# Performance work log

Measured on AMD Instinct MI355X. Metric: run time of the kernel, lower is better.

The kernel has to match this reference:

```python
import jax, jax.numpy as jnp
import numpy as np

B, Din, T, G = 8, 512, 1024, 128
DM, H, L, FF = 512, 8, 2, 2048
MAX_PERIOD = 10000.0


def _ln(x, s, b, eps=1e-5):
    m = x.mean(-1, keepdims=True)
    v = ((x - m) ** 2).mean(-1, keepdims=True)
    return (x - m) * jax.lax.rsqrt(v + eps) * s + b


def _rope(x, pos):
    # x: (B,H,S,Dh), pos: (S,)
    dh = x.shape[-1]
    half = dh // 2
    freqs = 1.0 / (MAX_PERIOD ** (jnp.arange(half, dtype=jnp.float32) / half))
    ang = pos[:, None] * freqs[None, :]              # (S, half)
    cos, sin = jnp.cos(ang), jnp.sin(ang)
    x1, x2 = x[..., :half], x[..., half:]
    return jnp.concatenate([x1 * cos - x2 * sin, x1 * sin + x2 * cos], axis=-1)


def _transformer(x, W_in, b_in, ln1_s, ln1_b, Wq, Wk, Wv, Wo, ls1,
                 ln2_s, ln2_b, W1, b1, W2, b2, ls2, lnf_s, lnf_b, W_out, b_out):
    # x: (B, Din, S) conv layout -> (B, S, DM)
    h = jnp.einsum('bds,de->bse', x, W_in) + b_in
    Bx, S, E = h.shape
    dh = E // H
    pos = jnp.arange(S, dtype=jnp.float32)
    scale = 1.0 / jnp.sqrt(jnp.asarray(dh, h.dtype))
    for l in range(Wq.shape[0]):
        y = _ln(h, ln1_s[l], ln1_b[l])
        q = (y @ Wq[l]).reshape(Bx, S, H, dh).transpose(0, 2, 1, 3)
        k = (y @ Wk[l]).reshape(Bx, S, H, dh).transpose(0, 2, 1, 3)
        v = (y @ Wv[l]).reshape(Bx, S, H, dh).transpose(0, 2, 1, 3)
        q, k = _rope(q, pos), _rope(k, pos)
        att = jax.nn.softmax(jnp.einsum('bhqd,bhkd->bhqk', q, k) * scale, axis=-1)
        o = jnp.einsum('bhqk,bhkd->bhqd', att, v).transpose(0, 2, 1, 3).reshape(Bx, S, E)
        h = h + ls1[l] * (o @ Wo[l])
        y = _ln(h, ln2_s[l], ln2_b[l])
        h = h + ls2[l] * (jax.nn.gelu(y @ W1[l] + b1[l]) @ W2[l] + b2[l])
    h = _ln(h, lnf_s, lnf_b)
    return (h @ W_out + b_out).transpose(0, 2, 1)  # (B, Din, S)


def _forward(features, alignment_matrix, num_segments_per_item, params):
    Bx, D, Tt = features.shape
    Gx = alignment_matrix.shape[1]
    ar_t = jnp.arange(Tt, dtype=jnp.int32)
    ar_g = jnp.arange(Gx, dtype=jnp.int32)
    group_mask = ar_g[None, :] < num_segments_per_item[:, None]          # (B,G)
    group_last = (alignment_matrix * ar_t.astype(features.dtype)).max(axis=2).astype(jnp.int32)  # (B,G)
    valid_last = jnp.where(group_mask, group_last, -1)
    frame_lengths = valid_last.max(axis=1) + 1                            # (B,)
    frame_mask = ar_t[None, :] < frame_lengths[:, None]                   # (B,T)
    last_for_count = jnp.where(group_mask, group_last, Tt + 1)
    num_q_before = jnp.sum(last_for_count[:, :, None] < ar_t[None, None, :], axis=1).astype(jnp.int32)  # (B,T)
    frame_dest = ar_t[None, :] + num_q_before                             # (B,T)
    query_dest = group_last + ar_g[None, :] + 1                           # (B,G)
    # mean-pooled query init
    summed = jnp.einsum('bgt,bdt->bgd', alignment_matrix, features)
    counts = jnp.maximum(alignment_matrix.sum(axis=2), 1.0)
    queries = (summed / counts[..., None]).transpose(0, 2, 1)             # (B,D,G)
    source_seq = jnp.concatenate([features, queries], axis=2)             # (B,D,T+G)
    dest = jnp.concatenate([frame_dest, query_dest], axis=1)              # (B,T+G)
    smask = jnp.concatenate([frame_mask, group_mask], axis=1)
    dest_m = jnp.where(smask, dest, Tt + Gx)
    perm = jnp.argsort(dest_m, axis=1)                                    # (B,T+G)
    interleaved = jnp.take_along_axis(source_seq, perm[:, None, :], axis=2)
    tout = _transformer(interleaved, *params)                             # (B,D,T+G)
    inv_perm = jnp.argsort(perm, axis=1)
    qpos = inv_perm[:, Tt:]                                               # (B,G)
    agg = jnp.take_along_axis(tout, qpos[:, None, :], axis=2)             # (B,D,G)
    return jnp.where(group_mask[:, None, :], agg, 0.0)


def setup_inputs() -> dict:
    key = jax.random.key(0)
    ks = jax.random.split(key, 8)
    rng = np.random.default_rng(0)
    align = np.zeros((B, G, T), np.float32)
    num_seg = np.zeros((B,), np.int32)
    for b in range(B):
        n = int(rng.integers(G // 2, G + 1))
        cuts = np.sort(rng.choice(np.arange(1, T), n - 1, replace=False))
        gid = np.searchsorted(cuts, np.arange(T), side='right')
        align[b, gid, np.arange(T)] = 1.0
        num_seg[b] = n
    s = 0.02
    return {
        'features': jax.random.normal(ks[0], (B, Din, T), jnp.float32),
        'alignment_matrix': jnp.asarray(align),
        'num_segments_per_item': jnp.asarray(num_seg),
        'W_in': jax.random.normal(ks[1], (Din, DM), jnp.float32) * s,
        'b_in': jnp.zeros((DM,), jnp.float32),
        'ln1_s': jnp.ones((L, DM), jnp.float32), 'ln1_b': jnp.zeros((L, DM), jnp.float32),
        'Wq': jax.random.normal(ks[2], (L, DM, DM), jnp.float32) * s,
        'Wk': jax.random.normal(ks[3], (L, DM, DM), jnp.float32) * s,
        'Wv': jax.random.normal(ks[4], (L, DM, DM), jnp.float32) * s,
        'Wo': jax.random.normal(ks[5], (L, DM, DM), jnp.float32) * s,
        'ls1': 0.01 * jnp.ones((L, DM), jnp.float32),
        'ln2_s': jnp.ones((L, DM), jnp.float32), 'ln2_b': jnp.zeros((L, DM), jnp.float32),
        'W1': jax.random.normal(ks[6], (L, DM, FF), jnp.float32) * s,
        'b1': jnp.zeros((L, FF), jnp.float32),
        'W2': jax.random.normal(ks[7], (L, FF, DM), jnp.float32) * s,
        'b2': jnp.zeros((L, DM), jnp.float32),
        'ls2': 0.01 * jnp.ones((L, DM), jnp.float32),
        'lnf_s': jnp.ones((DM,), jnp.float32), 'lnf_b': jnp.zeros((DM,), jnp.float32),
        'W_out': jax.random.normal(jax.random.fold_in(key, 9), (DM, Din), jnp.float32) * s,
        'b_out': jnp.zeros((Din,), jnp.float32),
    }


def reference(features, alignment_matrix, num_segments_per_item, W_in, b_in, ln1_s, ln1_b,
              Wq, Wk, Wv, Wo, ls1, ln2_s, ln2_b, W1, b1, W2, b2, ls2, lnf_s, lnf_b, W_out, b_out):
    params = (W_in, b_in, ln1_s, ln1_b, Wq, Wk, Wv, Wo, ls1,
              ln2_s, ln2_b, W1, b1, W2, b2, ls2, lnf_s, lnf_b, W_out, b_out)
    return _forward(features, alignment_matrix, num_segments_per_item, params)
```

## Files before the change

### kernel.cpp

```cpp
#include <hip/hip_runtime.h>
#include <hip/hip_bf16.h>
#include <math.h>

#define NB   8
#define NT   1024
#define NG   128
#define NS   1152
#define NDIN 512
#define NDM  512
#define NH   8
#define NDH  64
#define NFF  2048
#define NL   2

typedef __attribute__((ext_vector_type(4))) float  floatx4;
typedef __attribute__((ext_vector_type(8))) short  shortx8;

__device__ __forceinline__ float gelu_f(float x) {
    float u = 1.5957691216057308f * (x + 0.044715f * x * x * x);
    return x / (1.0f + __expf(-u));
}

__device__ __forceinline__ void gload_lds16(const void* g, void* l) {
    __builtin_amdgcn_global_load_lds((const __attribute__((address_space(1))) unsigned int*)g,
                                     (__attribute__((address_space(3))) unsigned int*)l, 16, 0, 0);
}

__device__ __forceinline__ short f2bfs(float x) {
    __hip_bfloat16 h = __float2bfloat16(x);
    return *(short*)&h;
}
__device__ __forceinline__ unsigned pack_bf2_rz(float a, float b) {
    unsigned au = *(unsigned*)&a, bu = *(unsigned*)&b;
    return (au >> 16) | (bu & 0xFFFF0000u);
}

__device__ __forceinline__ void swzxy(int& bx, int& by, int gx, int gy) {
    const int nwg = gx * gy;
    int flat = by * gx + bx;
    if ((nwg & 7) == 0) flat = (flat & 7) * (nwg >> 3) + (flat >> 3);
    bx = flat % gx; by = flat / gx;
}

__device__ __forceinline__ void wtile(const float* __restrict__ src,
        __hip_bfloat16* __restrict__ dst, int K, int N, int i, int tid, short tile[32][33])
{
    const int gx = N / 32;
    const int n0 = (i % gx) * 32;
    const int k0 = (i / gx) * 32;
    {
        const int r = tid >> 3, c4 = (tid & 7) * 4;
        float4 v = *(const float4*)&src[(size_t)(k0 + r) * N + n0 + c4];
        tile[c4 + 0][r] = f2bfs(v.x);
        tile[c4 + 1][r] = f2bfs(v.y);
        tile[c4 + 2][r] = f2bfs(v.z);
        tile[c4 + 3][r] = f2bfs(v.w);
    }
    __syncthreads();
    {
        const int r = tid >> 3, c4 = (tid & 7) * 4;
        short* dp = (short*)dst + (size_t)(n0 + r) * K + k0 + c4;
        short4 v;
        v.x = tile[r][c4 + 0]; v.y = tile[r][c4 + 1];
        v.z = tile[r][c4 + 2]; v.w = tile[r][c4 + 3];
        *(short4*)dp = v;
    }
}

__global__ __launch_bounds__(256) void prep0_k(
        float2* __restrict__ tab,
        const float* __restrict__ features, float* __restrict__ featT,
        const float* W_in, const float* Wq, const float* Wk, const float* Wv,
        const float* Wo, const float* W1, const float* W2, const float* W_out,
        __hip_bfloat16* w_inT, __hip_bfloat16* wqkvT0, __hip_bfloat16* wqkvT1,
        __hip_bfloat16* woT0, __hip_bfloat16* woT1,
        __hip_bfloat16* w1T0, __hip_bfloat16* w1T1,
        __hip_bfloat16* w2T0, __hip_bfloat16* w2T1, __hip_bfloat16* woutT)
{
    __shared__ __align__(16) char smem[32 * 33 * 4];
    const int tid = threadIdx.x;
    const int blk = blockIdx.x;
    if (blk < 144) {
        const int idx = blk * 256 + tid;
        const int s = idx >> 5, i = idx & 31;
        const float fr = __expf(-(float)i * 0.28782313662425576f);
        const float ang = (float)s * fr;
        tab[idx] = make_float2(cosf(ang), sinf(ang));
    } else if (blk < 144 + 4096) {
        float (*tile)[33] = (float(*)[33])smem;
        const int v = blk - 144;
        const int t0 = (v & 31) * 32;
        const int d0 = ((v >> 5) & 15) * 32;
        const int b  = v >> 9;
        const int r = tid >> 3, c4 = (tid & 7) * 4;
        {
            float4 w = *(const float4*)&features[((size_t)(b * NDIN + d0 + r)) * NT + t0 + c4];
            tile[c4 + 0][r] = w.x; tile[c4 + 1][r] = w.y;
            tile[c4 + 2][r] = w.z; tile[c4 + 3][r] = w.w;
        }
        __syncthreads();
        {
            float4 w;
            w.x = tile[r][c4 + 0]; w.y = tile[r][c4 + 1];
            w.z = tile[r][c4 + 2]; w.w = tile[r][c4 + 3];
            *(float4*)&featT[((size_t)(b * NT + t0 + r)) * NDIN + d0 + c4] = w;
        }
    } else {
        short (*tile)[33] = (short(*)[33])smem;
        const int i = blk - (144 + 4096);
        const float* src; __hip_bfloat16* dst; int K, N, ti;
        if (i < 256) { src = W_in; dst = w_inT; K = 512; N = 512; ti = i; }
        else if (i < 6400) {
            int r = i - 256;
            const int l = r / 3072; r -= l * 3072;
            const size_t o5 = (size_t)l * 262144, o2 = (size_t)l * 1048576;
            if (r < 256)       { src = Wq + o5; dst = (l ? wqkvT1 : wqkvT0);          K = 512;  N = 512;  ti = r; }
            else if (r < 512)  { src = Wk + o5; dst = (l ? wqkvT1 : wqkvT0) + 262144; K = 512;  N = 512;  ti = r - 256; }
            else if (r < 768)  { src = Wv + o5; dst = (l ? wqkvT1 : wqkvT0) + 524288; K = 512;  N = 512;  ti = r - 512; }
            else if (r < 1024) { src = Wo + o5; dst = (l ? woT1 : woT0);              K = 512;  N = 512;  ti = r - 768; }
            else if (r < 2048) { src = W1 + o2; dst = (l ? w1T1 : w1T0);              K = 512;  N = 2048; ti = r - 1024; }
            else               { src = W2 + o2; dst = (l ? w2T1 : w2T0);              K = 2048; N = 512;  ti = r - 2048; }
        }
        else { src = W_out; dst = woutT; K = 512; N = 512; ti = i - 6400; }
        wtile(src, dst, K, N, ti, tid, tile);
    }
}

__global__ __launch_bounds__(256) void pool_k(const float* __restrict__ align,
        const float* __restrict__ featT, int* __restrict__ glast,
        float* __restrict__ queries)
{
    __shared__ float redf[256];
    __shared__ int   redi[256];
    __shared__ float aw[NT];
    const int bg = blockIdx.x;
    const int b = bg >> 7;
    const int tid = threadIdx.x;
    const float* arow = align + (size_t)bg * NT;
    float cnt = 0.f, last = 0.f;
    int tmin = NT;
    for (int t = tid; t < NT; t += 256) {
        float a = arow[t];
        cnt += a;
        last = fmaxf(last, a * (float)t);
        if (a > 0.f) tmin = min(tmin, t);
    }
    redf[tid] = cnt; __syncthreads();
    for (int s = 128; s > 0; s >>= 1) { if (tid < s) redf[tid] += redf[tid + s]; __syncthreads(); }
    float c = redf[0]; __syncthreads();
    redf[tid] = last; __syncthreads();
    for (int s = 128; s > 0; s >>= 1) { if (tid < s) redf[tid] = fmaxf(redf[tid], redf[tid + s]); __syncthreads(); }
    float l = redf[0];
    redi[tid] = tmin; __syncthreads();
    for (int s = 128; s > 0; s >>= 1) { if (tid < s) redi[tid] = min(redi[tid], redi[tid + s]); __syncthreads(); }
    const int t0 = redi[0];
    const int t1 = (int)l;
    if (tid == 0) glast[bg] = t1;
    __syncthreads();
    for (int t = t0 + tid; t <= t1; t += 256) aw[t - t0] = arow[t];
    __syncthreads();
    const float invc = 1.0f / fmaxf(c, 1.0f);
    const float* fT = featT + (size_t)b * NT * NDIN;
    for (int d = tid; d < NDIN; d += 256) {
        float s = 0.f;
        for (int t = t0; t <= t1; ++t) s += aw[t - t0] * fT[(size_t)t * NDIN + d];
        queries[(size_t)bg * NDIN + d] = s * invc;
    }
}

__global__ __launch_bounds__(256) void rank_k(const int* __restrict__ glast,
        const int* __restrict__ nsegp, int* __restrict__ perm, int* __restrict__ qpos)
{
    __shared__ int dm[NS];
    __shared__ int gl[NG];
    const int b = blockIdx.y;
    const int tid = threadIdx.x;
    const int j = blockIdx.x * 256 + tid;
    if (tid < NG) gl[tid] = glast[b * NG + tid];
    const int ns = nsegp[b];
    __syncthreads();
    for (int jj = tid; jj < NS; jj += 256) {
        int d;
        if (jj < NT) {
            int t = jj, nq = 0, flen = 0;
            for (int g = 0; g < ns; ++g) {
                flen = max(flen, gl[g] + 1);
                nq += (gl[g] < t) ? 1 : 0;
            }
            d = (t < flen) ? (t + nq) : NS;
        } else {
            int g = jj - NT;
            d = (g < ns) ? (gl[g] + g + 1) : NS;
        }
        dm[jj] = d;
    }
    __syncthreads();
    if (j < NS) {
        const int my = dm[j];
        int r = 0;
        for (int t = 0; t < NS; ++t) {
            int v2 = dm[t];
            r += (v2 < my || (v2 == my && t < j)) ? 1 : 0;
        }
        perm[b * NS + r] = j;
        if (j >= NT) qpos[b * NG + (j - NT)] = r;
    }
}

__global__ __launch_bounds__(256) void buildx_k(const float* __restrict__ featT,
        const float* __restrict__ queries, const int* __restrict__ perm,
        __hip_bfloat16* __restrict__ X)
{
    const int idx = blockIdx.x * 256 + threadIdx.x;
    if (idx >= NB * NS * (NDIN / 4)) return;
    const int dq = idx & 127;
    const int p = (idx >> 7) % NS;
    const int b = idx / (NS * 128);
    const int j = perm[b * NS + p];
    const float4* src = (j < NT)
        ? (const float4*)&featT[((size_t)(b * NT + j)) * NDIN]
        : (const float4*)&queries[((size_t)(b * NG + (j - NT))) * NDIN];
    float4 v = src[dq];
    short4 o;
    o.x = f2bfs(v.x); o.y = f2bfs(v.y); o.z = f2bfs(v.z); o.w = f2bfs(v.w);
    *(short4*)((short*)X + ((size_t)(b * NS + p)) * NDIN + dq * 4) = o;
}

__global__ __launch_bounds__(256) void bgemmw1_k(const __hip_bfloat16* __restrict__ A,
        const __hip_bfloat16* __restrict__ Bt, __hip_bfloat16* __restrict__ Cout,
        const float* __restrict__ bias, int M, int N, int K)
{
    __shared__ __align__(16) short SM[4][128 * 32];
    const int tid = threadIdx.x;
    const int wave = tid >> 6, lane = tid & 63;
    const int quad = lane >> 4, l16 = lane & 15;
    const int wm = wave >> 1, wn = wave & 1;
    int bx = blockIdx.x, by = blockIdx.y;
    swzxy(bx, by, gridDim.x, gridDim.y);
    const size_t bm = (size_t)by * 128, bn = (size_t)bx * 128;
    const int sw = (l16 >> 1) & 3;
    const short* Ag = (const short*)A;
    const short* Bg = (const short*)Bt;
    const int lrow = lane >> 2;
    const int lchunk = (lane & 3) ^ ((lane >> 3) & 3);
    const int rS = wave * 32;

    floatx4 acc[4][4];
#pragma unroll
    for (int i = 0; i < 4; ++i)
#pragma unroll
        for (int j = 0; j < 4; ++j) acc[i][j] = (floatx4){0.f, 0.f, 0.f, 0.f};

    {
        const size_t ra = (bm + rS + lrow) * (size_t)K + lchunk * 8;
        const size_t rb = (bn + rS + lrow) * (size_t)K + lchunk * 8;
        gload_lds16(Ag + ra,                    &SM[0][rS * 32]);
        gload_lds16(Ag + ra + 16 * (size_t)K,   &SM[0][(rS + 16) * 32]);
        gload_lds16(Bg + rb,                    &SM[2][rS * 32]);
        gload_lds16(Bg + rb + 16 * (size_t)K,   &SM[2][(rS + 16) * 32]);
    }
    __syncthreads();
    int cur = 0;
    for (int k0 = 0; k0 < K; k0 += 32) {
        if (k0 + 32 < K) {
            const int nx = cur ^ 1;
            const size_t ra = (bm + rS + lrow) * (size_t)K + (k0 + 32) + lchunk * 8;
            const size_t rb = (bn + rS + lrow) * (size_t)K + (k0 + 32) + lchunk * 8;
            gload_lds16(Ag + ra,                  &SM[nx][rS * 32]);
            gload_lds16(Ag + ra + 16 * (size_t)K, &SM[nx][(rS + 16) * 32]);
            gload_lds16(Bg + rb,                  &SM[2 + nx][rS * 32]);
            gload_lds16(Bg + rb + 16 * (size_t)K, &SM[2 + nx][(rS + 16) * 32]);
        }
        shortx8 af[4], bf[4];
#pragma unroll
        for (int t = 0; t < 4; ++t) {
            af[t] = *(const shortx8*)&SM[cur][(wm * 64 + t * 16 + l16) * 32 + ((quad ^ sw) * 8)];
            bf[t] = *(const shortx8*)&SM[2 + cur][(wn * 64 + t * 16 + l16) * 32 + ((quad ^ sw) * 8)];
        }
#pragma unroll
        for (int mt = 0; mt < 4; ++mt)
#pragma unroll
            for (int nt = 0; nt < 4; ++nt)
                acc[mt][nt] = __builtin_amdgcn_mfma_f32_16x16x32_bf16(af[mt], bf[nt], acc[mt][nt], 0, 0, 0);
        __syncthreads();
        cur ^= 1;
    }
    const size_t mbase = bm + wm * 64;
    const size_t nbase = bn + wn * 64;
    short* ep = &SM[wave][0];
#pragma unroll
    for (int nt = 0; nt < 4; ++nt) {
        const size_t n = nbase + nt * 16 + l16;
        const float bz = bias[n];
        const int col = nt * 16 + l16;
#pragma unroll
        for (int mt = 0; mt < 4; ++mt)
#pragma unroll
            for (int r = 0; r < 4; ++r) {
                const int rl = mt * 16 + quad * 4 + r;
                float e = gelu_f(acc[mt][nt][r] + bz);
                ep[rl * 64 + (((col >> 3) ^ (rl & 7)) * 8) + (col & 7)] = f2bfs(e);
            }
    }
    __asm__ __volatile__("" ::: "memory");
#pragma unroll
    for (int c2 = 0; c2 < 8; ++c2) {
        const int rl = c2 * 8 + (lane >> 3);
        const int cc = lane & 7;
        shortx8 v = *(const shortx8*)&ep[rl * 64 + ((cc ^ (rl & 7)) * 8)];
        *(shortx8*)((short*)Cout + (mbase + rl) * N + nbase + cc * 8) = v;
    }
}

__global__ __launch_bounds__(256) void bgemmqkv_k(const __hip_bfloat16* __restrict__ A,
        const __hip_bfloat16* __restrict__ Bt, __hip_bfloat16* __restrict__ qh,
        __hip_bfloat16* __restrict__ kh, __hip_bfloat16* __restrict__ vT,
        const float2* __restrict__ tab)
{
    __shared__ __align__(16) short SM[4][128 * 32];
    const int tid = threadIdx.x;
    const int wave = tid >> 6, lane = tid & 63;
    const int quad = lane >> 4, l16 = lane & 15;
    const int wm = wave >> 1, wn = wave & 1;
    int bx = blockIdx.x, by = blockIdx.y;
    swzxy(bx, by, gridDim.x, gridDim.y);
    const size_t bm = (size_t)by * 128, bn = (size_t)bx * 128;
    const int sw = (l16 >> 1) & 3;
    const int K = 512;
    const short* Ag = (const short*)A;
    const short* Bg = (const short*)Bt;
    const int lrow = lane >> 2;
    const int lchunk = (lane & 3) ^ ((lane >> 3) & 3);
    const int rS = wave * 32;

    floatx4 acc[4][4];
#pragma unroll
    for (int i = 0; i < 4; ++i)
#pragma unroll
        for (int j = 0; j < 4; ++j) acc[i][j] = (floatx4){0.f, 0.f, 0.f, 0.f};

    {
        const size_t ra = (bm + rS + lrow) * (size_t)K + lchunk * 8;
        const size_t rb = (bn + rS + lrow) * (size_t)K + lchunk * 8;
        gload_lds16(Ag + ra,                  &SM[0][rS * 32]);
        gload_lds16(Ag + ra + 16 * (size_t)K, &SM[0][(rS + 16) * 32]);
        gload_lds16(Bg + rb,                  &SM[2][rS * 32]);
        gload_lds16(Bg + rb + 16 * (size_t)K, &SM[2][(rS + 16) * 32]);
    }
    __syncthreads();
    int cur = 0;
    for (int k0 = 0; k0 < K; k0 += 32) {
        if (k0 + 32 < K) {
            const int nx = cur ^ 1;
            const size_t ra = (bm + rS + lrow) * (size_t)K + (k0 + 32) + lchunk * 8;
            const size_t rb = (bn + rS + lrow) * (size_t)K + (k0 + 32) + lchunk * 8;
            gload_lds16(Ag + ra,                  &SM[nx][rS * 32]);
            gload_lds16(Ag + ra + 16 * (size_t)K, &SM[nx][(rS + 16) * 32]);
            gload_lds16(Bg + rb,                  &SM[2 + nx][rS * 32]);
            gload_lds16(Bg + rb + 16 * (size_t)K, &SM[2 + nx][(rS + 16) * 32]);
        }
        shortx8 af[4], bf[4];
#pragma unroll
        for (int t = 0; t < 4; ++t) {
            af[t] = *(const shortx8*)&SM[cur][(wm * 64 + t * 16 + l16) * 32 + ((quad ^ sw) * 8)];
            bf[t] = *(const shortx8*)&SM[2 + cur][(wn * 64 + t * 16 + l16) * 32 + ((quad ^ sw) * 8)];
        }
#pragma unroll
        for (int mt = 0; mt < 4; ++mt)
#pragma unroll
            for (int nt = 0; nt < 4; ++nt)
                acc[mt][nt] = __builtin_amdgcn_mfma_f32_16x16x32_bf16(af[mt], bf[nt], acc[mt][nt], 0, 0, 0);
        __syncthreads();
        cur ^= 1;
    }
    short* ep = &SM[wave][0];
    const int bidx = (int)(bm / NS);
    const int sbase = (int)(bm - (size_t)bidx * NS) + wm * 64;
    const int region = (int)(bn >> 9);
    if (region < 2) {
        const float qsc = region ? 1.0f : 0.18033688011112043f;
        const int h = (int)((((int)bn & 511) + wn * 64) >> 6);
#pragma unroll
        for (int nt = 0; nt < 2; ++nt) {
            const int d1 = nt * 16 + l16, d2 = d1 + 32;
            const float2* tp = tab + d1;
#pragma unroll
            for (int mt = 0; mt < 4; ++mt)
#pragma unroll
                for (int r = 0; r < 4; ++r) {
                    const int sl = mt * 16 + quad * 4 + r;
                    const int s = sbase + sl;
                    float x1 = acc[mt][nt][r], x2 = acc[mt][nt + 2][r];
                    float2 cs = tp[s * 32];
                    ep[sl * 64 + (((d1 >> 3) ^ (sl & 7)) * 8) + (d1 & 7)] = f2bfs(qsc * (x1 * cs.x - x2 * cs.y));
                    ep[sl * 64 + (((d2 >> 3) ^ (sl & 7)) * 8) + (d2 & 7)] = f2bfs(qsc * (x1 * cs.y + x2 * cs.x));
                }
        }
        __asm__ __volatile__("" ::: "memory");
        short* dst = (short*)(region ? kh : qh) + ((size_t)(bidx * NH + h)) * NS * NDH;
#pragma unroll
        for (int c2 = 0; c2 < 8; ++c2) {
            const int sl = c2 * 8 + (lane >> 3);
            const int cc = lane & 7;
            shortx8 v = *(const shortx8*)&ep[sl * 64 + ((cc ^ (sl & 7)) * 8)];
            *(shortx8*)(dst + (size_t)(sbase + sl) * NDH + cc * 8) = v;
        }
    } else {
        const int base = (int)(bn - 1024) + wn * 64;
        const int h = base >> 6;
#pragma unroll
        for (int nt = 0; nt < 4; ++nt) {
            const int dl = nt * 16 + l16;
#pragma unroll
            for (int mt = 0; mt < 4; ++mt)
#pragma unroll
                for (int r = 0; r < 4; ++r) {
                    const int sl = mt * 16 + quad * 4 + r;
                    ep[dl * 64 + (((sl >> 3) ^ (dl & 7)) * 8) + (sl & 7)] = f2bfs(acc[mt][nt][r]);
                }
        }
        __asm__ __volatile__("" ::: "memory");
        short* vp = (short*)vT + ((size_t)(bidx * NH + h)) * NDH * NS;
#pragma unroll
        for (int c2 = 0; c2 < 8; ++c2) {
            const int dl = c2 * 8 + (lane >> 3);
            const int cc = lane & 7;
            shortx8 v = *(const shortx8*)&ep[dl * 64 + ((cc ^ (dl & 7)) * 8)];
            *(shortx8*)(vp + (size_t)dl * NS + sbase + cc * 8) = v;
        }
    }
}

template <int EPI>
__global__ __launch_bounds__(256) void bgemm64_k(const __hip_bfloat16* __restrict__ A,
        const __hip_bfloat16* __restrict__ Bt, void* __restrict__ Cout,
        const float* __restrict__ bias, const float* __restrict__ ls,
        const float* __restrict__ res, const int* __restrict__ nsegp, int M, int N, int K)
{
    __shared__ __align__(16) short As[2][64 * 32];
    __shared__ __align__(16) short Bs[2][128 * 32];
    const int tid = threadIdx.x;
    const int wave = tid >> 6, lane = tid & 63;
    const int quad = lane >> 4, l16 = lane & 15;
    const int wm = wave >> 1, wn = wave & 1;
    int bx = blockIdx.x, by = blockIdx.y;
    swzxy(bx, by, gridDim.x, gridDim.y);
    const size_t bm = (size_t)by * 64, bn = (size_t)bx * 128;
    const int sw = (l16 >> 1) & 3;
    const short* Ag = (const short*)A;
    const short* Bg = (const short*)Bt;
    const int lrow = lane >> 2;
    const int lchunk = (lane & 3) ^ ((lane >> 3) & 3);
    const int rA = wave * 16, rB = wave * 32;

    floatx4 acc[2][4];
#pragma unroll
    for (int i = 0; i < 2; ++i)
#pragma unroll
        for (int j = 0; j < 4; ++j) acc[i][j] = (floatx4){0.f, 0.f, 0.f, 0.f};

    {
        const size_t ra = (bm + rA + lrow) * (size_t)K + lchunk * 8;
        const size_t rb = (bn + rB + lrow) * (size_t)K + lchunk * 8;
        gload_lds16(Ag + ra,                  &As[0][rA * 32]);
        gload_lds16(Bg + rb,                  &Bs[0][rB * 32]);
        gload_lds16(Bg + rb + 16 * (size_t)K, &Bs[0][(rB + 16) * 32]);
    }
    __syncthreads();
    int cur = 0;
    for (int k0 = 0; k0 < K; k0 += 32) {
        if (k0 + 32 < K) {
            const int nx = cur ^ 1;
            const size_t ra = (bm + rA + lrow) * (size_t)K + (k0 + 32) + lchunk * 8;
            const size_t rb = (bn + rB + lrow) * (size_t)K + (k0 + 32) + lchunk * 8;
            gload_lds16(Ag + ra,                  &As[nx][rA * 32]);
            gload_lds16(Bg + rb,                  &Bs[nx][rB * 32]);
            gload_lds16(Bg + rb + 16 * (size_t)K, &Bs[nx][(rB + 16) * 32]);
        }
        shortx8 af[2], bf[4];
#pragma unroll
        for (int t = 0; t < 2; ++t)
            af[t] = *(const shortx8*)&As[cur][(wm * 32 + t * 16 + l16) * 32 + ((quad ^ sw) * 8)];
#pragma unroll
        for (int t = 0; t < 4; ++t)
            bf[t] = *(const shortx8*)&Bs[cur][(wn * 64 + t * 16 + l16) * 32 + ((quad ^ sw) * 8)];
#pragma unroll
        for (int mt = 0; mt < 2; ++mt)
#pragma unroll
            for (int nt = 0; nt < 4; ++nt)
                acc[mt][nt] = __builtin_amdgcn_mfma_f32_16x16x32_bf16(af[mt], bf[nt], acc[mt][nt], 0, 0, 0);
        __syncthreads();
        cur ^= 1;
    }
    const size_t mbase = bm + wm * 32;
    const size_t nbase = bn + wn * 64;
#pragma unroll
    for (int nt = 0; nt < 4; ++nt) {
        const size_t n = nbase + nt * 16 + l16;
        const float bz = bias ? bias[n] : 0.f;
        const float lz = (EPI == 2) ? ls[n] : 0.f;
#pragma unroll
        for (int mt = 0; mt < 2; ++mt) {
#pragma unroll
            for (int r = 0; r < 4; ++r) {
                const size_t m = mbase + mt * 16 + quad * 4 + r;
                float e = acc[mt][nt][r] + bz;
                if (EPI == 4) {
                    const int b = (int)(m >> 7), g = (int)(m & 127);
                    float val = (g < nsegp[b]) ? e : 0.0f;
                    ((float*)Cout)[(size_t)b * (NDIN * NG) + n * NG + g] = val;
                } else {
                    const size_t off = m * N + n;
                    if (EPI == 2) e = res[off] + lz * e;
                    ((float*)Cout)[off] = e;
                }
            }
        }
    }
}

__global__ __launch_bounds__(256) void lnw_k(const float* __restrict__ in,
        __hip_bfloat16* __restrict__ out, const float* __restrict__ gam, const float* __restrict__ bet)
{
    const int r = blockIdx.x * 4 + (threadIdx.x >> 6);
    const int t = threadIdx.x & 63;
    const float4* xp = (const float4*)(in + (size_t)r * NDM);
    float4 a = xp[t * 2], b4 = xp[t * 2 + 1];
    float s = a.x + a.y + a.z + a.w + b4.x + b4.y + b4.z + b4.w;
#pragma unroll
    for (int o = 1; o < 64; o <<= 1) s += __shfl_xor(s, o);
    const float mean = s * (1.0f / NDM);
    float dx[8] = {a.x - mean, a.y - mean, a.z - mean, a.w - mean,
                   b4.x - mean, b4.y - mean, b4.z - mean, b4.w - mean};
    float v = 0.f;
#pragma unroll
    for (int i = 0; i < 8; ++i) v += dx[i] * dx[i];
#pragma unroll
    for (int o = 1; o < 64; o <<= 1) v += __shfl_xor(v, o);
    const float inv = rsqrtf(v * (1.0f / NDM) + 1e-5f);
    const float4* gp = (const float4*)gam;
    const float4* bp = (const float4*)bet;
    float4 g0 = gp[t * 2], g1 = gp[t * 2 + 1], q0 = bp[t * 2], q1 = bp[t * 2 + 1];
    shortx8 o8;
    o8[0] = f2bfs(dx[0] * inv * g0.x + q0.x);
    o8[1] = f2bfs(dx[1] * inv * g0.y + q0.y);
    o8[2] = f2bfs(dx[2] * inv * g0.z + q0.z);
    o8[3] = f2bfs(dx[3] * inv * g0.w + q0.w);
    o8[4] = f2bfs(dx[4] * inv * g1.x + q1.x);
    o8[5] = f2bfs(dx[5] * inv * g1.y + q1.y);
    o8[6] = f2bfs(dx[6] * inv * g1.z + q1.z);
    o8[7] = f2bfs(dx[7] * inv * g1.w + q1.w);
    *(shortx8*)((short*)out + (size_t)r * NDM + t * 8) = o8;
}

__global__ __launch_bounds__(64) void lnwg_k(const float* __restrict__ h,
        __hip_bfloat16* __restrict__ out, const float* __restrict__ gam, const float* __restrict__ bet,
        const int* __restrict__ qpos)
{
    const int r = blockIdx.x, t = threadIdx.x;
    const int b = r >> 7;
    const int src = qpos[r];
    const float4* xp = (const float4*)(h + ((size_t)(b * NS + src)) * NDM);
    float4 a = xp[t * 2], b4 = xp[t * 2 + 1];
    float s = a.x + a.y + a.z + a.w + b4.x + b4.y + b4.z + b4.w;
#pragma unroll
    for (int o = 1; o < 64; o <<= 1) s += __shfl_xor(s, o);
    const float mean = s * (1.0f / NDM);
    float dx[8] = {a.x - mean, a.y - mean, a.z - mean, a.w - mean,
                   b4.x - mean, b4.y - mean, b4.z - mean, b4.w - mean};
    float v = 0.f;
#pragma unroll
    for (int i = 0; i < 8; ++i) v += dx[i] * dx[i];
#pragma unroll
    for (int o = 1; o < 64; o <<= 1) v += __shfl_xor(v, o);
    const float inv = rsqrtf(v * (1.0f / NDM) + 1e-5f);
    const float4* gp = (const float4*)gam;
    const float4* bp = (const float4*)bet;
    float4 g0 = gp[t * 2], g1 = gp[t * 2 + 1], q0 = bp[t * 2], q1 = bp[t * 2 + 1];
    shortx8 o8;
    o8[0] = f2bfs(dx[0] * inv * g0.x + q0.x);
    o8[1] = f2bfs(dx[1] * inv * g0.y + q0.y);
    o8[2] = f2bfs(dx[2] * inv * g0.z + q0.z);
    o8[3] = f2bfs(dx[3] * inv * g0.w + q0.w);
    o8[4] = f2bfs(dx[4] * inv * g1.x + q1.x);
    o8[5] = f2bfs(dx[5] * inv * g1.y + q1.y);
    o8[6] = f2bfs(dx[6] * inv * g1.z + q1.z);
    o8[7] = f2bfs(dx[7] * inv * g1.w + q1.w);
    *(shortx8*)((short*)out + (size_t)r * NDM + t * 8) = o8;
}

#define FKT 64
#define FKP 68
#define NTL (NS / FKT)
__global__ __launch_bounds__(256) void fattn_k(const __hip_bfloat16* __restrict__ qb,
        const __hip_bfloat16* __restrict__ kb, const __hip_bfloat16* __restrict__ vbT,
        __hip_bfloat16* __restrict__ o)
{
    __shared__ __align__(16) short Ks[FKT * FKP];
    __shared__ __align__(16) short Vt[(NDH + 16) * FKP];
    __shared__ __align__(16) short Pl[64 * FKP];
    const int tid = threadIdx.x;
    const int wave = tid >> 6, lane = tid & 63;
    const int quad = lane >> 4, l16 = lane & 15;
    const int L = blockIdx.x;
    const int xcd = L & 7, sl = L >> 3;
    const int bh = (xcd << 3) | (sl & 7);
    const int q0 = (sl >> 3) * 64;
    const int bb = bh >> 3, hh = bh & 7;
    const short* qbase = (const short*)qb + (size_t)bh * NS * NDH;
    const short* kbase = (const short*)kb + (size_t)bh * NS * NDH;
    const short* vbase = (const short*)vbT + (size_t)bh * NDH * NS;

    shortx8 Qf0, Qf1;
    {
        const short* qp = qbase + (size_t)(q0 + wave * 16 + l16) * NDH + quad * 8;
        Qf0 = *(const shortx8*)qp;
        Qf1 = *(const shortx8*)(qp + 32);
    }
    {
        const int rr = 64 + (tid >> 4);
        const int cc = (tid & 15) * 4;
        short4 ones; ones.x = 0x3F80; ones.y = 0x3F80; ones.z = 0x3F80; ones.w = 0x3F80;
        *(short4*)&Vt[rr * FKP + cc] = ones;
    }
    __syncthreads();
    shortx8 Of0 = *(const shortx8*)&Vt[(64 + l16) * FKP + quad * 8];
    shortx8 Of1 = *(const shortx8*)&Vt[(64 + l16) * FKP + 32 + quad * 8];

    floatx4 Oacc[4];
#pragma unroll
    for (int i = 0; i < 4; ++i) Oacc[i] = (floatx4){0.f, 0.f, 0.f, 0.f};
    floatx4 Oacc5 = (floatx4){0.f, 0.f, 0.f, 0.f};

    const int sr = tid >> 2, sc = (tid & 3) * 16;
    const int prow = wave * 16 + l16;
    const short* kg = kbase + (size_t)sr * NDH + sc;
    const short* vg = vbase + (size_t)sr * NS + sc;
    shortx8 pk0 = *(const shortx8*)kg, pk1 = *(const shortx8*)(kg + 8);
    shortx8 pv0 = *(const shortx8*)vg, pv1 = *(const shortx8*)(vg + 8);

    for (int t = 0; t < NTL; ++t) {
        __syncthreads();
        *(shortx8*)&Ks[sr * FKP + sc]     = pk0;
        *(shortx8*)&Ks[sr * FKP + sc + 8] = pk1;
        *(shortx8*)&Vt[sr * FKP + sc]     = pv0;
        *(shortx8*)&Vt[sr * FKP + sc + 8] = pv1;
        __syncthreads();
        if (t + 1 < NTL) {
            kg += FKT * NDH; vg += FKT;
            pk0 = *(const shortx8*)kg; pk1 = *(const shortx8*)(kg + 8);
            pv0 = *(const shortx8*)vg; pv1 = *(const shortx8*)(vg + 8);
        }

        floatx4 S[4];
#pragma unroll
        for (int kbk = 0; kbk < 4; ++kbk) {
            shortx8 kf0 = *(const shortx8*)&Ks[(kbk * 16 + l16) * FKP + quad * 8];
            shortx8 kf1 = *(const shortx8*)&Ks[(kbk * 16 + l16) * FKP + 32 + quad * 8];
            floatx4 sa = (floatx4){0.f, 0.f, 0.f, 0.f};
            sa = __builtin_amdgcn_mfma_f32_16x16x32_bf16(kf0, Qf0, sa, 0, 0, 0);
            sa = __builtin_amdgcn_mfma_f32_16x16x32_bf16(kf1, Qf1, sa, 0, 0, 0);
            S[kbk] = sa;
        }
#pragma unroll
        for (int kbk = 0; kbk < 4; ++kbk) {
            uint2 u;
            u.x = pack_bf2_rz(exp2f(S[kbk][0]), exp2f(S[kbk][1]));
            u.y = pack_bf2_rz(exp2f(S[kbk][2]), exp2f(S[kbk][3]));
            *(uint2*)&Pl[prow * FKP + kbk * 16 + quad * 4] = u;
        }
        __asm__ __volatile__("" ::: "memory");
        shortx8 Pf0 = *(const shortx8*)&Pl[prow * FKP + quad * 8];
        shortx8 Pf1 = *(const shortx8*)&Pl[prow * FKP + 32 + quad * 8];
#pragma unroll
        for (int ct = 0; ct < 4; ++ct) {
            shortx8 vf0 = *(const shortx8*)&Vt[(ct * 16 + l16) * FKP + quad * 8];
            shortx8 vf1 = *(const shortx8*)&Vt[(ct * 16 + l16) * FKP + 32 + quad * 8];
            Oacc[ct] = __builtin_amdgcn_mfma_f32_16x16x32_bf16(Pf0, vf0, Oacc[ct], 0, 0, 0);
            Oacc[ct] = __builtin_amdgcn_mfma_f32_16x16x32_bf16(Pf1, vf1, Oacc[ct], 0, 0, 0);
        }
        Oacc5 = __builtin_amdgcn_mfma_f32_16x16x32_bf16(Pf0, Of0, Oacc5, 0, 0, 0);
        Oacc5 = __builtin_amdgcn_mfma_f32_16x16x32_bf16(Pf1, Of1, Oacc5, 0, 0, 0);
    }
    float lr[4];
#pragma unroll
    for (int i = 0; i < 4; ++i) lr[i] = __shfl(Oacc5[i], quad * 16);
#pragma unroll
    for (int i = 0; i < 4; ++i) {
        const float inv = 1.0f / lr[i];
        const int row = q0 + wave * 16 + quad * 4 + i;
        __hip_bfloat16* op = o + ((size_t)(bb * NS + row)) * NDM + hh * NDH + l16;
        op[0]  = __float2bfloat16(Oacc[0][i] * inv);
        op[16] = __float2bfloat16(Oacc[1][i] * inv);
        op[32] = __float2bfloat16(Oacc[2][i] * inv);
        op[48] = __float2bfloat16(Oacc[3][i] * inv);
    }
}

extern "C" void kernel_launch(void* const* d_in, const int* in_sizes, int n_in,
                              void* d_out, int out_size, void* d_ws, size_t ws_size,
                              hipStream_t stream) {
    const float* features = (const float*)d_in[0];
    const float* align    = (const float*)d_in[1];
    const int*   nseg     = (const int*)d_in[2];
    const float* W_in  = (const float*)d_in[3];
    const float* b_in  = (const float*)d_in[4];
    const float* ln1_s = (const float*)d_in[5];
    const float* ln1_b = (const float*)d_in[6];
    const float* Wq = (const float*)d_in[7];
    const float* Wk = (const float*)d_in[8];
    const float* Wv = (const float*)d_in[9];
    const float* Wo = (const float*)d_in[10];
    const float* ls1   = (const float*)d_in[11];
    const float* ln2_s = (const float*)d_in[12];
    const float* ln2_b = (const float*)d_in[13];
    const float* W1 = (const float*)d_in[14];
    const float* b1 = (const float*)d_in[15];
    const float* W2 = (const float*)d_in[16];
    const float* b2 = (const float*)d_in[17];
    const float* ls2   = (const float*)d_in[18];
    const float* lnf_s = (const float*)d_in[19];
    const float* lnf_b = (const float*)d_in[20];
    const float* W_out = (const float*)d_in[21];
    const float* b_out = (const float*)d_in[22];

    const size_t SZ_BSD = (size_t)NB * NS * NDM;

    float* p = (float*)d_ws;
    __hip_bfloat16* w_inT  = (__hip_bfloat16*)p;
    __hip_bfloat16* wqkvT0 = w_inT + 512 * 512;
    __hip_bfloat16* wqkvT1 = wqkvT0 + 1536 * 512;
    __hip_bfloat16* woT0   = wqkvT1 + 1536 * 512;
    __hip_bfloat16* woT1   = woT0 + 512 * 512;
    __hip_bfloat16* w1T0   = woT1 + 512 * 512;
    __hip_bfloat16* w1T1   = w1T0 + 2048 * 512;
    __hip_bfloat16* w2T0   = w1T1 + 2048 * 512;
    __hip_bfloat16* w2T1   = w2T0 + 512 * 2048;
    __hip_bfloat16* woutT  = w2T1 + 512 * 2048;
    int* glast = (int*)(woutT + 512 * 512);
    int* perm  = glast + NB * NG;
    int* qpos  = perm + NB * NS;
    float2* ropetab = (float2*)(qpos + NB * NG);
    p = (float*)(ropetab + NS * 32);

    float* featT = p; p += (size_t)NB * NT * NDIN;
    float* hbuf = p; p += SZ_BSD;
    __hip_bfloat16* ybuf = (__hip_bfloat16*)p;  p += SZ_BSD / 2;
    __hip_bfloat16* obuf = (__hip_bfloat16*)p;  p += SZ_BSD / 2;
    __hip_bfloat16* ubuf = (__hip_bfloat16*)p;  p += SZ_BSD * 2;
    __hip_bfloat16* xin  = (__hip_bfloat16*)p;  p += SZ_BSD / 2;
    float* quer = p; p += (size_t)NB * NG * NDIN;
    __hip_bfloat16* hq = (__hip_bfloat16*)p; p += (size_t)NB * NG * NDM / 2;
    const size_t needed = (size_t)((char*)p - (char*)d_ws);
    if (ws_size < needed) return;

    __hip_bfloat16* qh = ubuf;
    __hip_bfloat16* kh = ubuf + SZ_BSD;
    __hip_bfloat16* vT = xin;

    prep0_k<<<144 + 4096 + 6656, 256, 0, stream>>>(ropetab, features, featT,
            W_in, Wq, Wk, Wv, Wo, W1, W2, W_out,
            w_inT, wqkvT0, wqkvT1, woT0, woT1, w1T0, w1T1, w2T0, w2T1, woutT);
    pool_k<<<NB * NG, 256, 0, stream>>>(align, featT, glast, quer);
    rank_k<<<dim3((NS + 255) / 256, NB), 256, 0, stream>>>(glast, nseg, perm, qpos);
    buildx_k<<<(NB * NS * (NDIN / 4) + 255) / 256, 256, 0, stream>>>(featT, quer, perm, xin);

    const int M = NB * NS;
    bgemm64_k<0><<<dim3(NDM / 128, M / 64), 256, 0, stream>>>(xin, w_inT, hbuf, b_in, nullptr, nullptr, nullptr, M, NDM, NDIN);

    for (int l = 0; l < NL; ++l) {
        __hip_bfloat16* wqkvT = (l ? wqkvT1 : wqkvT0);
        __hip_bfloat16* woT   = (l ? woT1 : woT0);
        __hip_bfloat16* w1T   = (l ? w1T1 : w1T0);
        __hip_bfloat16* w2T   = (l ? w2T1 : w2T0);

        lnw_k<<<M / 4, 256, 0, stream>>>(hbuf, ybuf, ln1_s + l * NDM, ln1_b + l * NDM);
        bgemmqkv_k<<<dim3(1536 / 128, M / 128), 256, 0, stream>>>(ybuf, wqkvT, qh, kh, vT, ropetab);
        fattn_k<<<(NS / 64) * NH * NB, 256, 0, stream>>>(qh, kh, vT, obuf);
        bgemm64_k<2><<<dim3(NDM / 128, M / 64), 256, 0, stream>>>(obuf, woT, hbuf, nullptr, ls1 + l * NDM, hbuf, nullptr, M, NDM, NDM);
        lnw_k<<<M / 4, 256, 0, stream>>>(hbuf, ybuf, ln2_s + l * NDM, ln2_b + l * NDM);
        bgemmw1_k<<<dim3(NFF / 128, M / 128), 256, 0, stream>>>(ybuf, w1T, ubuf, b1 + l * NFF, M, NFF, NDM);
        bgemm64_k<2><<<dim3(NDM / 128, M / 64), 256, 0, stream>>>(ubuf, w2T, hbuf, b2 + l * NDM, ls2 + l * NDM, hbuf, nullptr, M, NDM, NFF);
    }

    lnwg_k<<<NB * NG, 64, 0, stream>>>(hbuf, hq, lnf_s, lnf_b, qpos);
    bgemm64_k<4><<<dim3(NDIN / 128, (NB * NG) / 64), 256, 0, stream>>>(hq, woutT, d_out, b_out, nullptr, nullptr, nseg, NB * NG, NDIN, NDM);
}
```

Baseline: 608.6 us.

## Software-pipeline QK^T one tile ahead in flash attention with MFMA priority hints

Restructures the attention inner loop so the QK^T scores for the next key tile are computed in the same iteration as the exp and PV of the current tile. This lets MFMA work overlap the softmax exponentials, and s_setprio raises wave priority around the MFMA blocks. The all-ones row-sum operand is now built in registers instead of staged through LDS, which drops one barrier and the LDS padding rows. Using the same ones fragment for both halves also makes the row sum available in every lane, so the final shuffle goes away. The cost is extra register pressure for the second score buffer and more complex buffer indexing.

```diff
diff --git a/kernel.cpp b/kernel.cpp
--- a/kernel.cpp
+++ b/kernel.cpp
@@ -597,7 +597,7 @@
         __hip_bfloat16* __restrict__ o)
 {
     __shared__ __align__(16) short Ks[FKT * FKP];
-    __shared__ __align__(16) short Vt[(NDH + 16) * FKP];
+    __shared__ __align__(16) short Vt[NDH * FKP];
     __shared__ __align__(16) short Pl[64 * FKP];
     const int tid = threadIdx.x;
     const int wave = tid >> 6, lane = tid & 63;
@@ -617,15 +617,9 @@
         Qf0 = *(const shortx8*)qp;
         Qf1 = *(const shortx8*)(qp + 32);
     }
-    {
-        const int rr = 64 + (tid >> 4);
-        const int cc = (tid & 15) * 4;
-        short4 ones; ones.x = 0x3F80; ones.y = 0x3F80; ones.z = 0x3F80; ones.w = 0x3F80;
-        *(short4*)&Vt[rr * FKP + cc] = ones;
-    }
-    __syncthreads();
-    shortx8 Of0 = *(const shortx8*)&Vt[(64 + l16) * FKP + quad * 8];
-    shortx8 Of1 = *(const shortx8*)&Vt[(64 + l16) * FKP + 32 + quad * 8];
+    shortx8 Of;
+#pragma unroll
+    for (int i = 0; i < 8; ++i) Of[i] = 0x3F80;
 
     floatx4 Oacc[4];
 #pragma unroll
@@ -636,31 +630,54 @@
     const int prow = wave * 16 + l16;
     const short* kg = kbase + (size_t)sr * NDH + sc;
     const short* vg = vbase + (size_t)sr * NS + sc;
+
     shortx8 pk0 = *(const shortx8*)kg, pk1 = *(const shortx8*)(kg + 8);
     shortx8 pv0 = *(const shortx8*)vg, pv1 = *(const shortx8*)(vg + 8);
-
+    *(shortx8*)&Ks[sr * FKP + sc]     = pk0;
+    *(shortx8*)&Ks[sr * FKP + sc + 8] = pk1;
+    kg += FKT * NDH;
+    pk0 = *(const shortx8*)kg; pk1 = *(const shortx8*)(kg + 8);
+    __syncthreads();
+
+    floatx4 S[4], Sn[4];
+#pragma unroll
+    for (int kbk = 0; kbk < 4; ++kbk) {
+        shortx8 kf0 = *(const shortx8*)&Ks[(kbk * 16 + l16) * FKP + quad * 8];
+        shortx8 kf1 = *(const shortx8*)&Ks[(kbk * 16 + l16) * FKP + 32 + quad * 8];
+        floatx4 sa = (floatx4){0.f, 0.f, 0.f, 0.f};
+        sa = __builtin_amdgcn_mfma_f32_16x16x32_bf16(kf0, Qf0, sa, 0, 0, 0);
+        sa = __builtin_amdgcn_mfma_f32_16x16x32_bf16(kf1, Qf1, sa, 0, 0, 0);
+        S[kbk] = sa;
+    }
+
+#pragma unroll 2
     for (int t = 0; t < NTL; ++t) {
         __syncthreads();
-        *(shortx8*)&Ks[sr * FKP + sc]     = pk0;
-        *(shortx8*)&Ks[sr * FKP + sc + 8] = pk1;
+        if (t + 1 < NTL) {
+            *(shortx8*)&Ks[sr * FKP + sc]     = pk0;
+            *(shortx8*)&Ks[sr * FKP + sc + 8] = pk1;
+        }
         *(shortx8*)&Vt[sr * FKP + sc]     = pv0;
         *(shortx8*)&Vt[sr * FKP + sc + 8] = pv1;
         __syncthreads();
         if (t + 1 < NTL) {
-            kg += FKT * NDH; vg += FKT;
-            pk0 = *(const shortx8*)kg; pk1 = *(const shortx8*)(kg + 8);
+            if (t + 2 < NTL) {
+                kg += FKT * NDH;
+                pk0 = *(const shortx8*)kg; pk1 = *(const shortx8*)(kg + 8);
+            }
+            vg += FKT;
             pv0 = *(const shortx8*)vg; pv1 = *(const shortx8*)(vg + 8);
-        }
-
-        floatx4 S[4];
-#pragma unroll
-        for (int kbk = 0; kbk < 4; ++kbk) {
-            shortx8 kf0 = *(const shortx8*)&Ks[(kbk * 16 + l16) * FKP + quad * 8];
-            shortx8 kf1 = *(const shortx8*)&Ks[(kbk * 16 + l16) * FKP + 32 + quad * 8];
-            floatx4 sa = (floatx4){0.f, 0.f, 0.f, 0.f};
-            sa = __builtin_amdgcn_mfma_f32_16x16x32_bf16(kf0, Qf0, sa, 0, 0, 0);
-            sa = __builtin_amdgcn_mfma_f32_16x16x32_bf16(kf1, Qf1, sa, 0, 0, 0);
-            S[kbk] = sa;
+            __builtin_amdgcn_s_setprio(1);
+#pragma unroll
+            for (int kbk = 0; kbk < 4; ++kbk) {
+                shortx8 kf0 = *(const shortx8*)&Ks[(kbk * 16 + l16) * FKP + quad * 8];
+                shortx8 kf1 = *(const shortx8*)&Ks[(kbk * 16 + l16) * FKP + 32 + quad * 8];
+                floatx4 sa = (floatx4){0.f, 0.f, 0.f, 0.f};
+                sa = __builtin_amdgcn_mfma_f32_16x16x32_bf16(kf0, Qf0, sa, 0, 0, 0);
+                sa = __builtin_amdgcn_mfma_f32_16x16x32_bf16(kf1, Qf1, sa, 0, 0, 0);
+                Sn[kbk] = sa;
+            }
+            __builtin_amdgcn_s_setprio(0);
         }
 #pragma unroll
         for (int kbk = 0; kbk < 4; ++kbk) {
@@ -672,6 +689,7 @@
         __asm__ __volatile__("" ::: "memory");
         shortx8 Pf0 = *(const shortx8*)&Pl[prow * FKP + quad * 8];
         shortx8 Pf1 = *(const shortx8*)&Pl[prow * FKP + 32 + quad * 8];
+        __builtin_amdgcn_s_setprio(1);
 #pragma unroll
         for (int ct = 0; ct < 4; ++ct) {
             shortx8 vf0 = *(const shortx8*)&Vt[(ct * 16 + l16) * FKP + quad * 8];
@@ -679,15 +697,15 @@
             Oacc[ct] = __builtin_amdgcn_mfma_f32_16x16x32_bf16(Pf0, vf0, Oacc[ct], 0, 0, 0);
             Oacc[ct] = __builtin_amdgcn_mfma_f32_16x16x32_bf16(Pf1, vf1, Oacc[ct], 0, 0, 0);
         }
-        Oacc5 = __builtin_amdgcn_mfma_f32_16x16x32_bf16(Pf0, Of0, Oacc5, 0, 0, 0);
-        Oacc5 = __builtin_amdgcn_mfma_f32_16x16x32_bf16(Pf1, Of1, Oacc5, 0, 0, 0);
-    }
-    float lr[4];
-#pragma unroll
-    for (int i = 0; i < 4; ++i) lr[i] = __shfl(Oacc5[i], quad * 16);
+        Oacc5 = __builtin_amdgcn_mfma_f32_16x16x32_bf16(Pf0, Of, Oacc5, 0, 0, 0);
+        Oacc5 = __builtin_amdgcn_mfma_f32_16x16x32_bf16(Pf1, Of, Oacc5, 0, 0, 0);
+        __builtin_amdgcn_s_setprio(0);
+#pragma unroll
+        for (int i = 0; i < 4; ++i) S[i] = Sn[i];
+    }
 #pragma unroll
     for (int i = 0; i < 4; ++i) {
-        const float inv = 1.0f / lr[i];
+        const float inv = 1.0f / Oacc5[i];
         const int row = q0 + wave * 16 + quad * 4 + i;
         __hip_bfloat16* op = o + ((size_t)(bb * NS + row)) * NDM + hh * NDH + l16;
         op[0]  = __float2bfloat16(Oacc[0][i] * inv);
```

Result: no change. 602.1 us (-1.1%).

## Widen flash-attention query tile to 128 rows with 512-thread blocks

Applied to the files above, without the earlier changes.

The attention kernel now handles 128 query rows per block with 8 waves instead of 64 rows with 4 waves. Each K/V tile staged in LDS is therefore reused by twice as many queries, and each thread loads half as much per tile. The all-ones operand used for the row-sum MFMA is now built in registers rather than in LDS, which removes a barrier and a shuffle. It also raises wave priority around the PV MFMAs with s_setprio. The trade-off is half as many blocks and larger blocks, which may hurt occupancy and load balance.

```diff
diff --git a/kernel.cpp b/kernel.cpp
--- a/kernel.cpp
+++ b/kernel.cpp
@@ -592,20 +592,21 @@
 #define FKT 64
 #define FKP 68
 #define NTL (NS / FKT)
-__global__ __launch_bounds__(256) void fattn_k(const __hip_bfloat16* __restrict__ qb,
+#define QB  128
+__global__ __launch_bounds__(512) void fattn_k(const __hip_bfloat16* __restrict__ qb,
         const __hip_bfloat16* __restrict__ kb, const __hip_bfloat16* __restrict__ vbT,
         __hip_bfloat16* __restrict__ o)
 {
     __shared__ __align__(16) short Ks[FKT * FKP];
-    __shared__ __align__(16) short Vt[(NDH + 16) * FKP];
-    __shared__ __align__(16) short Pl[64 * FKP];
+    __shared__ __align__(16) short Vt[NDH * FKP];
+    __shared__ __align__(16) short Pl[QB * FKP];
     const int tid = threadIdx.x;
     const int wave = tid >> 6, lane = tid & 63;
     const int quad = lane >> 4, l16 = lane & 15;
     const int L = blockIdx.x;
     const int xcd = L & 7, sl = L >> 3;
     const int bh = (xcd << 3) | (sl & 7);
-    const int q0 = (sl >> 3) * 64;
+    const int q0 = (sl >> 3) * QB;
     const int bb = bh >> 3, hh = bh & 7;
     const short* qbase = (const short*)qb + (size_t)bh * NS * NDH;
     const short* kbase = (const short*)kb + (size_t)bh * NS * NDH;
@@ -617,39 +618,31 @@
         Qf0 = *(const shortx8*)qp;
         Qf1 = *(const shortx8*)(qp + 32);
     }
-    {
-        const int rr = 64 + (tid >> 4);
-        const int cc = (tid & 15) * 4;
-        short4 ones; ones.x = 0x3F80; ones.y = 0x3F80; ones.z = 0x3F80; ones.w = 0x3F80;
-        *(short4*)&Vt[rr * FKP + cc] = ones;
-    }
-    __syncthreads();
-    shortx8 Of0 = *(const shortx8*)&Vt[(64 + l16) * FKP + quad * 8];
-    shortx8 Of1 = *(const shortx8*)&Vt[(64 + l16) * FKP + 32 + quad * 8];
+    shortx8 Of;
+#pragma unroll
+    for (int i = 0; i < 8; ++i) Of[i] = 0x3F80;
 
     floatx4 Oacc[4];
 #pragma unroll
     for (int i = 0; i < 4; ++i) Oacc[i] = (floatx4){0.f, 0.f, 0.f, 0.f};
     floatx4 Oacc5 = (floatx4){0.f, 0.f, 0.f, 0.f};
 
-    const int sr = tid >> 2, sc = (tid & 3) * 16;
+    const int sr = tid >> 3, sc = (tid & 7) * 8;
     const int prow = wave * 16 + l16;
     const short* kg = kbase + (size_t)sr * NDH + sc;
     const short* vg = vbase + (size_t)sr * NS + sc;
-    shortx8 pk0 = *(const shortx8*)kg, pk1 = *(const shortx8*)(kg + 8);
-    shortx8 pv0 = *(const shortx8*)vg, pv1 = *(const shortx8*)(vg + 8);
+    shortx8 pk = *(const shortx8*)kg;
+    shortx8 pv = *(const shortx8*)vg;
 
     for (int t = 0; t < NTL; ++t) {
         __syncthreads();
-        *(shortx8*)&Ks[sr * FKP + sc]     = pk0;
-        *(shortx8*)&Ks[sr * FKP + sc + 8] = pk1;
-        *(shortx8*)&Vt[sr * FKP + sc]     = pv0;
-        *(shortx8*)&Vt[sr * FKP + sc + 8] = pv1;
+        *(shortx8*)&Ks[sr * FKP + sc] = pk;
+        *(shortx8*)&Vt[sr * FKP + sc] = pv;
         __syncthreads();
         if (t + 1 < NTL) {
             kg += FKT * NDH; vg += FKT;
-            pk0 = *(const shortx8*)kg; pk1 = *(const shortx8*)(kg + 8);
-            pv0 = *(const shortx8*)vg; pv1 = *(const shortx8*)(vg + 8);
+            pk = *(const shortx8*)kg;
+            pv = *(const shortx8*)vg;
         }
 
         floatx4 S[4];
@@ -672,6 +665,7 @@
         __asm__ __volatile__("" ::: "memory");
         shortx8 Pf0 = *(const shortx8*)&Pl[prow * FKP + quad * 8];
         shortx8 Pf1 = *(const shortx8*)&Pl[prow * FKP + 32 + quad * 8];
+        __builtin_amdgcn_s_setprio(1);
 #pragma unroll
         for (int ct = 0; ct < 4; ++ct) {
             shortx8 vf0 = *(const shortx8*)&Vt[(ct * 16 + l16) * FKP + quad * 8];
@@ -679,15 +673,13 @@
             Oacc[ct] = __builtin_amdgcn_mfma_f32_16x16x32_bf16(Pf0, vf0, Oacc[ct], 0, 0, 0);
             Oacc[ct] = __builtin_amdgcn_mfma_f32_16x16x32_bf16(Pf1, vf1, Oacc[ct], 0, 0, 0);
         }
-        Oacc5 = __builtin_amdgcn_mfma_f32_16x16x32_bf16(Pf0, Of0, Oacc5, 0, 0, 0);
-        Oacc5 = __builtin_amdgcn_mfma_f32_16x16x32_bf16(Pf1, Of1, Oacc5, 0, 0, 0);
-    }
-    float lr[4];
-#pragma unroll
-    for (int i = 0; i < 4; ++i) lr[i] = __shfl(Oacc5[i], quad * 16);
+        Oacc5 = __builtin_amdgcn_mfma_f32_16x16x32_bf16(Pf0, Of, Oacc5, 0, 0, 0);
+        Oacc5 = __builtin_amdgcn_mfma_f32_16x16x32_bf16(Pf1, Of, Oacc5, 0, 0, 0);
+        __builtin_amdgcn_s_setprio(0);
+    }
 #pragma unroll
     for (int i = 0; i < 4; ++i) {
-        const float inv = 1.0f / lr[i];
+        const float inv = 1.0f / Oacc5[i];
         const int row = q0 + wave * 16 + quad * 4 + i;
         __hip_bfloat16* op = o + ((size_t)(bb * NS + row)) * NDM + hh * NDH + l16;
         op[0]  = __float2bfloat16(Oacc[0][i] * inv);
@@ -776,7 +768,7 @@
 
         lnw_k<<<M / 4, 256, 0, stream>>>(hbuf, ybuf, ln1_s + l * NDM, ln1_b + l * NDM);
         bgemmqkv_k<<<dim3(1536 / 128, M / 128), 256, 0, stream>>>(ybuf, wqkvT, qh, kh, vT, ropetab);
-        fattn_k<<<(NS / 64) * NH * NB, 256, 0, stream>>>(qh, kh, vT, obuf);
+        fattn_k<<<(NS / QB) * NH * NB, 512, 0, stream>>>(qh, kh, vT, obuf);
         bgemm64_k<2><<<dim3(NDM / 128, M / 64), 256, 0, stream>>>(obuf, woT, hbuf, nullptr, ls1 + l * NDM, hbuf, nullptr, M, NDM, NDM);
         lnw_k<<<M / 4, 256, 0, stream>>>(hbuf, ybuf, ln2_s + l * NDM, ln2_b + l * NDM);
         bgemmw1_k<<<dim3(NFF / 128, M / 128), 256, 0, stream>>>(ybuf, w1T, ubuf, b1 + l * NFF, M, NFF, NDM);
```

After: 601.2 us, median of 3. No clear change (-1.2%).
